# Kernel tuning notes

Hardware: AMD Instinct MI355X
Metric: run time of the kernel (lower is better)

Reference implementation:

```python
import jax, jax.numpy as jnp
import numpy as np

B, S, D, H, DK = 2, 2048, 2048, 16, 128
ALIBI_SLOPE = 8.0
NEG = -1e9  # finite stand-in for -inf so gradients stay finite


def setup_inputs() -> dict:
    key = jax.random.key(0)
    ks = jax.random.split(key, 8)
    states = jax.random.normal(ks[0], (B, S, D), jnp.float32)
    # causal ALiBi-style additive bias: -(i-j) for j<=i else very negative
    pos = jnp.arange(S)
    dist = pos[None, :] - pos[:, None]  # j - i
    bias = jnp.where(dist <= 0, dist.astype(jnp.float32), NEG)
    bias_mask = jnp.broadcast_to(bias[None], (B, S, S))
    # per-head scale: exp2(-((h+1)*slope/H))
    head_scale = jnp.exp2(-((jnp.arange(H) + 1.0) * ALIBI_SLOPE / H)).astype(jnp.float32)
    init = lambda k, shp: jax.random.normal(k, shp, jnp.float32) * (shp[-1] ** -0.5)
    return {
        'states': states,
        'bias_mask': bias_mask,
        'head_scale': head_scale,
        'Wq': init(ks[1], (D, D)), 'bq': jnp.zeros((D,), jnp.float32),
        'Wk': init(ks[2], (D, D)), 'bk': jnp.zeros((D,), jnp.float32),
        'Wv': init(ks[3], (D, D)), 'bv': jnp.zeros((D,), jnp.float32),
        'Wg': init(ks[4], (H, D)), 'bg': jnp.zeros((H,), jnp.float32),
        'Wo': init(ks[5], (D, D)), 'bo': jnp.zeros((D,), jnp.float32),
    }


def reference(states, bias_mask, head_scale, Wq, bq, Wk, bk, Wv, bv, Wg, bg, Wo, bo):
    b, s, d = states.shape
    key_scale = DK ** -0.5
    proj = lambda x, W, bias: x @ W.T + bias
    # [b,s,d] -> [b,h,s,dk]
    q = proj(states, Wq, bq).reshape(b, s, H, DK).transpose(0, 2, 1, 3)
    k = proj(states, Wk, bk).reshape(b, s, H, DK).transpose(0, 2, 1, 3)
    v = proj(states, Wv, bv).reshape(b, s, H, DK).transpose(0, 2, 1, 3)
    # additive per-head ALiBi bias: [b,1,s,s] * [1,h,1,1]
    bias = bias_mask[:, None, :, :] * head_scale[None, :, None, None]
    scores = jnp.einsum('bhqd,bhkd->bhqk', q, k) * key_scale + bias
    attn = jax.nn.softmax(scores, axis=-1)
    o = jnp.einsum('bhqk,bhkd->bhqd', attn, v).transpose(0, 2, 1, 3)  # [b,s,h,dk]
    g = jax.nn.sigmoid(proj(states, Wg, bg))  # [b,s,h]
    o = o * g[..., None]
    return proj(o.reshape(b, s, d), Wo, bo)
```

## Files before the change

kernel.cpp:

```cpp
#include <hip/hip_runtime.h>

#define SEQ  2048
#define NROW 4096
#define KDIM 2048
#define NH   16
#define DKH  128
#define CSUB 20.0f
#define LOG2E 1.44269504088896f

typedef unsigned int u32;
typedef unsigned short u16;
typedef __attribute__((ext_vector_type(8))) __bf16 bf16x8;
typedef __attribute__((ext_vector_type(4))) float f32x4;
typedef __attribute__((ext_vector_type(4))) u16 u16x4;

struct alignas(16) U4 { u32 x, y, z, w; };

__device__ __forceinline__ u16 f2bf(float f) {
  u32 u = __builtin_bit_cast(u32, f);
  u32 r = (u + 0x7fffu + ((u >> 16) & 1u)) >> 16;
  return (u16)r;
}
__device__ __forceinline__ u16 f2bf_n(float f) {
  __bf16 h = (__bf16)f;
  return __builtin_bit_cast(u16, h);
}
__device__ __forceinline__ bf16x8 asb(U4 v) { return __builtin_bit_cast(bf16x8, v); }
__device__ __forceinline__ float exp2a(float x) {
  float r;
  asm("v_exp_f32 %0, %1" : "=v"(r) : "v"(x));
  return r;
}

__device__ __forceinline__ void gl2lds16(const u16* g, u16* l) {
  __builtin_amdgcn_global_load_lds(
      (const __attribute__((address_space(1))) void*)g,
      (__attribute__((address_space(3))) void*)l, 16, 0, 0);
}

__global__ __launch_bounds__(256)
void cvtk(const float* __restrict__ src, u16* __restrict__ dst, int n)
{
  const int i = (blockIdx.x * 256 + threadIdx.x) * 4;
  if (i < n) {
    f32x4 v = *(const f32x4*)(src + i);
    u16x4 o;
#pragma unroll
    for (int j = 0; j < 4; ++j) o[j] = f2bf_n(v[j]);
    *(u16x4*)(dst + i) = o;
  }
}

__global__ __launch_bounds__(256)
void cvt3k(const float* __restrict__ s0, const float* __restrict__ s1,
           const float* __restrict__ s2, u16* __restrict__ dst, int n)
{
  const float* s = blockIdx.y == 0 ? s0 : (blockIdx.y == 1 ? s1 : s2);
  u16* d = dst + (size_t)blockIdx.y * n;
  const int i = (blockIdx.x * 256 + threadIdx.x) * 4;
  if (i < n) {
    f32x4 v = *(const f32x4*)(s + i);
    u16x4 o;
#pragma unroll
    for (int j = 0; j < 4; ++j) o[j] = f2bf_n(v[j]);
    *(u16x4*)(d + i) = o;
  }
}

__device__ __forceinline__ void stage_ab(const u16* __restrict__ A,
                                         const u16* __restrict__ B,
                                         int m0, int n0, int kk,
                                         u16* Asb, u16* Bsb,
                                         int wave, int gr, int gc)
{
#pragma unroll
  for (int it = 0; it < 2; ++it) {
    const int r0 = wave * 32 + it * 16;
    gl2lds16(A + (size_t)(m0 + r0 + gr) * KDIM + kk + gc, Asb + r0 * 32);
    gl2lds16(B + (size_t)(n0 + r0 + gr) * KDIM + kk + gc, Bsb + r0 * 32);
  }
}

__global__ __launch_bounds__(256, 2)
void qkvg(const u16* __restrict__ A, const u16* __restrict__ B,
          const float* __restrict__ bq, const float* __restrict__ bk,
          const float* __restrict__ bv, u16* __restrict__ Qw,
          u16* __restrict__ Kw, u16* __restrict__ Vw)
{
  __shared__ alignas(16) u16 As[2][128 * 32];
  __shared__ alignas(16) u16 Bs[2][128 * 32];
  const int tid = threadIdx.x;
  const int lane = tid & 63, wave = tid >> 6;
  const int wm = wave >> 1, wn = wave & 1;
  const int l15 = lane & 15, quad = lane >> 4;
  const int m0 = blockIdx.y * 128, n0 = blockIdx.x * 128;

  f32x4 acc[4][4];
#pragma unroll
  for (int i = 0; i < 4; ++i)
#pragma unroll
    for (int j = 0; j < 4; ++j) acc[i][j] = {0.f, 0.f, 0.f, 0.f};

  const int gr = lane >> 2;
  const int gc = (lane & 3) * 8;

  stage_ab(A, B, m0, n0, 0, As[0], Bs[0], wave, gr, gc);

  const int NKI = KDIM / 32;
  for (int ki = 0; ki < NKI; ++ki) {
    const int cb = ki & 1;
    __syncthreads();
    if (ki + 1 < NKI)
      stage_ab(A, B, m0, n0, (ki + 1) * 32, As[cb ^ 1], Bs[cb ^ 1], wave, gr, gc);
    U4 af[4], bg[4];
#pragma unroll
    for (int t = 0; t < 4; ++t) {
      af[t] = *(const U4*)(As[cb] + (wm * 64 + t * 16 + l15) * 32 + quad * 8);
      bg[t] = *(const U4*)(Bs[cb] + (wn * 64 + t * 16 + l15) * 32 + quad * 8);
    }
#pragma unroll
    for (int mt = 0; mt < 4; ++mt)
#pragma unroll
      for (int nt = 0; nt < 4; ++nt)
        acc[mt][nt] = __builtin_amdgcn_mfma_f32_16x16x32_bf16(
            asb(af[mt]), asb(bg[nt]), acc[mt][nt], 0, 0, 0);
  }

  const int seg = n0 >> 11;
  const float* bp = seg == 0 ? bq : (seg == 1 ? bk : bv);
  u16* Cq = seg == 0 ? Qw : Kw;

#pragma unroll
  for (int mt = 0; mt < 4; ++mt) {
    const int rowb = m0 + wm * 64 + mt * 16 + quad * 4;
    const int b = rowb >> 11, srow = rowb & (SEQ - 1);
#pragma unroll
    for (int nt = 0; nt < 4; ++nt) {
      const int col6 = n0 + wn * 64 + nt * 16 + l15;
      const int col = col6 & 2047;
      const int h = col >> 7, dk = col & 127;
      const float bvl = bp[col];
      if (seg == 2) {
        u16x4 pk;
#pragma unroll
        for (int r = 0; r < 4; ++r) pk[r] = f2bf_n(acc[mt][nt][r] + bvl);
        const size_t idx = ((size_t)(b * NH + h) * DKH + dk) * SEQ + srow;
        *(u16x4*)(Vw + idx) = pk;
      } else {
#pragma unroll
        for (int r = 0; r < 4; ++r) {
          const size_t idx = ((size_t)(b * NH + h) * SEQ + (srow + r)) * DKH + dk;
          Cq[idx] = f2bf_n(acc[mt][nt][r] + bvl);
        }
      }
    }
  }
}

__global__ __launch_bounds__(256, 2)
void gemm_bt(const u16* __restrict__ A, const u16* __restrict__ B,
             const float* __restrict__ bias, float* __restrict__ Cf)
{
  __shared__ alignas(16) u16 As[2][128 * 32];
  __shared__ alignas(16) u16 Bs[2][128 * 32];
  const int tid = threadIdx.x;
  const int lane = tid & 63, wave = tid >> 6;
  const int wm = wave >> 1, wn = wave & 1;
  const int l15 = lane & 15, quad = lane >> 4;
  const int m0 = blockIdx.y * 128, n0 = blockIdx.x * 128;

  f32x4 acc[4][4];
#pragma unroll
  for (int i = 0; i < 4; ++i)
#pragma unroll
    for (int j = 0; j < 4; ++j) acc[i][j] = {0.f, 0.f, 0.f, 0.f};

  const int gr = lane >> 2;
  const int gc = (lane & 3) * 8;

  stage_ab(A, B, m0, n0, 0, As[0], Bs[0], wave, gr, gc);

  const int NKI = KDIM / 32;
  for (int ki = 0; ki < NKI; ++ki) {
    const int cb = ki & 1;
    __syncthreads();
    if (ki + 1 < NKI)
      stage_ab(A, B, m0, n0, (ki + 1) * 32, As[cb ^ 1], Bs[cb ^ 1], wave, gr, gc);
    U4 af[4], bg[4];
#pragma unroll
    for (int t = 0; t < 4; ++t) {
      af[t] = *(const U4*)(As[cb] + (wm * 64 + t * 16 + l15) * 32 + quad * 8);
      bg[t] = *(const U4*)(Bs[cb] + (wn * 64 + t * 16 + l15) * 32 + quad * 8);
    }
#pragma unroll
    for (int mt = 0; mt < 4; ++mt)
#pragma unroll
      for (int nt = 0; nt < 4; ++nt)
        acc[mt][nt] = __builtin_amdgcn_mfma_f32_16x16x32_bf16(
            asb(af[mt]), asb(bg[nt]), acc[mt][nt], 0, 0, 0);
  }

#pragma unroll
  for (int mt = 0; mt < 4; ++mt) {
    const int rowb = m0 + wm * 64 + mt * 16 + quad * 4;
#pragma unroll
    for (int nt = 0; nt < 4; ++nt) {
      const int col = n0 + wn * 64 + nt * 16 + l15;
      const float bv = bias[col];
#pragma unroll
      for (int r = 0; r < 4; ++r)
        Cf[(size_t)(rowb + r) * KDIM + col] = acc[mt][nt][r] + bv;
    }
  }
}

__global__ __launch_bounds__(256)
void gateg(const u16* __restrict__ X, const float* __restrict__ Wg,
           const float* __restrict__ bg, float* __restrict__ G)
{
  __shared__ float red[4][16][16];
  const int tid = threadIdx.x;
  const int lane = tid & 63, wave = tid >> 6;
  const int l15 = lane & 15, quad = lane >> 4;
  const int m0 = blockIdx.x * 16;

  const u16*  Xp = X + (size_t)(m0 + l15) * KDIM + wave * 512 + quad * 8;
  const float* Wp = Wg + (size_t)l15 * KDIM + wave * 512 + quad * 8;

  f32x4 acc = {0.f, 0.f, 0.f, 0.f};
#pragma unroll
  for (int kk = 0; kk < 512; kk += 32) {
    U4 a = *(const U4*)(Xp + kk);
    f32x4 w0 = *(const f32x4*)(Wp + kk);
    f32x4 w1 = *(const f32x4*)(Wp + kk + 4);
    U4 bw;
    bw.x = (u32)f2bf_n(w0[0]) | ((u32)f2bf_n(w0[1]) << 16);
    bw.y = (u32)f2bf_n(w0[2]) | ((u32)f2bf_n(w0[3]) << 16);
    bw.z = (u32)f2bf_n(w1[0]) | ((u32)f2bf_n(w1[1]) << 16);
    bw.w = (u32)f2bf_n(w1[2]) | ((u32)f2bf_n(w1[3]) << 16);
    acc = __builtin_amdgcn_mfma_f32_16x16x32_bf16(asb(a), asb(bw), acc, 0, 0, 0);
  }
#pragma unroll
  for (int r = 0; r < 4; ++r) red[wave][quad * 4 + r][l15] = acc[r];
  __syncthreads();
  const int row = tid >> 4, head = tid & 15;
  float s = bg[head];
#pragma unroll
  for (int w = 0; w < 4; ++w) s += red[w][row][head];
  G[(size_t)(m0 + row) * NH + head] = 1.f / (1.f + __expf(-s));
}

__device__ __forceinline__ void stage_kv(const u16* __restrict__ Kh,
                                         const u16* __restrict__ Vh,
                                         int kk, u16* Ksb, u16* Vsb,
                                         int wave, int lane)
{
  const int rK = lane >> 4, cK = lane & 15;
  const int rV = lane >> 3, cV = lane & 7;
#pragma unroll
  for (int j = 0; j < 4; ++j) {
    const int r0k = wave * 16 + j * 4;
    const int xk = ((j & 1) << 2) | rK;
    gl2lds16(Kh + (size_t)(kk + r0k + rK) * DKH + ((cK ^ xk) * 8),
             Ksb + r0k * 128);
    const int r0v = wave * 32 + j * 8;
    gl2lds16(Vh + (size_t)(r0v + rV) * SEQ + kk + ((cV ^ rV) * 8),
             Vsb + r0v * 64);
  }
}

__global__ __launch_bounds__(256, 2)
void attnk(const u16* __restrict__ Q, const u16* __restrict__ Km,
           const u16* __restrict__ Vt, const float* __restrict__ hsc,
           const float* __restrict__ G, u16* __restrict__ O)
{
  __shared__ alignas(16) u16 Ks[2][64 * 128];
  __shared__ alignas(16) u16 Vs[2][128 * 64];
  __shared__ alignas(16) u16 Ps[4][16 * 72];
  const int tid = threadIdx.x;
  const int lane = tid & 63, wave = tid >> 6;
  const int l15 = lane & 15, quad = lane >> 4;
  const int l7x = l15 & 7;
  const int qt = 31 - blockIdx.y, bh = blockIdx.x;
  const int b = bh >> 4, h = bh & 15;
  const size_t hoff = (size_t)bh * SEQ * DKH;
  const u16* Qh = Q + hoff;
  const u16* Kh = Km + hoff;
  const u16* Vh = Vt + hoff;
  const float hs2 = hsc[h] * LOG2E;
  const float ks2 = 0.08838834764831845f * LOG2E;
  const float csub2 = CSUB * LOG2E;
  const float dstep = 64.0f * hs2;

  const int q0 = qt * 64 + wave * 16;
  const int ntile = qt + 1;

  U4 aq[4];
#pragma unroll
  for (int c = 0; c < 4; ++c)
    aq[c] = *(const U4*)(Qh + (size_t)(q0 + l15) * DKH + c * 32 + quad * 8);

  float base[4][4];
#pragma unroll
  for (int r = 0; r < 4; ++r) {
    const int i = q0 + quad * 4 + r;
#pragma unroll
    for (int nt = 0; nt < 4; ++nt)
      base[r][nt] = (float)(nt * 16 + l15 - i) * hs2 - csub2;
  }

  f32x4 oacc[8];
#pragma unroll
  for (int c = 0; c < 8; ++c) oacc[c] = {0.f, 0.f, 0.f, 0.f};
  float l_lane[4] = {0.f, 0.f, 0.f, 0.f};

  stage_kv(Kh, Vh, 0, Ks[0], Vs[0], wave, lane);

  for (int t = 0; t < ntile; ++t) {
    const int kk = t * 64;
    const int cb = t & 1;
    __syncthreads();
    if (t + 1 < ntile)
      stage_kv(Kh, Vh, kk + 64, Ks[cb ^ 1], Vs[cb ^ 1], wave, lane);

    f32x4 sf[4];
#pragma unroll
    for (int nt = 0; nt < 4; ++nt) {
      f32x4 s = {0.f, 0.f, 0.f, 0.f};
#pragma unroll
      for (int c = 0; c < 4; ++c) {
        U4 bk = *(const U4*)(Ks[cb] + (nt * 16 + l15) * 128 +
                             (((c * 4 + quad) ^ l7x) * 8));
        s = __builtin_amdgcn_mfma_f32_16x16x32_bf16(asb(aq[c]), asb(bk), s, 0, 0, 0);
      }
      sf[nt] = s;
    }

    u16* Pw = &Ps[wave][0];
    const float tf = (float)t;
    if (t + 1 < ntile) {
#pragma unroll
      for (int r = 0; r < 4; ++r) {
#pragma unroll
        for (int nt = 0; nt < 4; ++nt) {
          const float p = exp2a(fmaf(sf[nt][r], ks2, fmaf(tf, dstep, base[r][nt])));
          l_lane[r] += p;
          Pw[(quad * 4 + r) * 72 + nt * 16 + l15] = f2bf_n(p);
        }
      }
    } else {
#pragma unroll
      for (int r = 0; r < 4; ++r) {
        const int i = q0 + quad * 4 + r;
#pragma unroll
        for (int nt = 0; nt < 4; ++nt) {
          const int j = kk + nt * 16 + l15;
          float p = 0.f;
          if (j <= i)
            p = exp2a(fmaf(sf[nt][r], ks2, fmaf(tf, dstep, base[r][nt])));
          l_lane[r] += p;
          Pw[(quad * 4 + r) * 72 + nt * 16 + l15] = f2bf_n(p);
        }
      }
    }
    asm volatile("s_waitcnt lgkmcnt(0)" ::: "memory");
    __builtin_amdgcn_sched_barrier(0);
    U4 pf0 = *(const U4*)(Pw + l15 * 72 + quad * 8);
    U4 pf1 = *(const U4*)(Pw + l15 * 72 + 32 + quad * 8);
#pragma unroll
    for (int c = 0; c < 8; ++c) {
      U4 bv0 = *(const U4*)(Vs[cb] + (c * 16 + l15) * 64 + ((quad ^ l7x) * 8));
      U4 bv1 = *(const U4*)(Vs[cb] + (c * 16 + l15) * 64 + (((quad + 4) ^ l7x) * 8));
      oacc[c] = __builtin_amdgcn_mfma_f32_16x16x32_bf16(asb(pf0), asb(bv0), oacc[c], 0, 0, 0);
      oacc[c] = __builtin_amdgcn_mfma_f32_16x16x32_bf16(asb(pf1), asb(bv1), oacc[c], 0, 0, 0);
    }
  }

  float sc[4];
#pragma unroll
  for (int r = 0; r < 4; ++r) {
#pragma unroll
    for (int d = 1; d < 16; d <<= 1)
      l_lane[r] += __shfl_xor(l_lane[r], d, 64);
    const int i = q0 + quad * 4 + r;
    sc[r] = G[(size_t)(b * SEQ + i) * NH + h] / l_lane[r];
  }

  __syncthreads();
  u16* OL = &Ks[0][0] + wave * 2112;
#pragma unroll
  for (int c = 0; c < 8; ++c)
#pragma unroll
    for (int r = 0; r < 4; ++r)
      OL[(quad * 4 + r) * 132 + c * 16 + l15] = f2bf_n(oacc[c][r] * sc[r]);
  __syncthreads();
#pragma unroll
  for (int o = 0; o < 4; ++o) {
    const int row = o * 4 + quad;
    U4 val = *(const U4*)(OL + row * 132 + l15 * 8);
    *(U4*)(O + ((size_t)(b * SEQ + q0 + row) * NH + h) * DKH + l15 * 8) = val;
  }
}

extern "C" void kernel_launch(void* const* d_in, const int* in_sizes, int n_in,
                              void* d_out, int out_size, void* d_ws, size_t ws_size,
                              hipStream_t stream)
{
  const float* states = (const float*)d_in[0];
  const float* hscale = (const float*)d_in[2];
  const float* Wq = (const float*)d_in[3];
  const float* bq = (const float*)d_in[4];
  const float* Wk = (const float*)d_in[5];
  const float* bk = (const float*)d_in[6];
  const float* Wv = (const float*)d_in[7];
  const float* bv = (const float*)d_in[8];
  const float* Wg = (const float*)d_in[9];
  const float* bg = (const float*)d_in[10];
  const float* Wo = (const float*)d_in[11];
  const float* bo = (const float*)d_in[12];
  float* out = (float*)d_out;

  char* ws = (char*)d_ws;
  const size_t MB = 1024 * 1024;
  u16* S16  = (u16*)(ws);
  u16* Qw   = (u16*)(ws + 16 * MB);
  u16* Kw   = (u16*)(ws + 32 * MB);
  u16* Vw   = (u16*)(ws + 48 * MB);
  u16* W16  = (u16*)(ws + 64 * MB);
  u16* Ow   = (u16*)(ws + 64 * MB);
  u16* Wo16 = (u16*)(ws + 80 * MB);
  float* Gw = out;

  const int NW = KDIM * KDIM;
  const int NS = NROW * KDIM;
  dim3 blk(256);

  cvtk<<<dim3(NS / 1024), blk, 0, stream>>>(states, S16, NS);
  gateg<<<dim3(NROW / 16), blk, 0, stream>>>(S16, Wg, bg, Gw);
  cvt3k<<<dim3(NW / 1024, 3), blk, 0, stream>>>(Wq, Wk, Wv, W16, NW);
  qkvg<<<dim3(48, 32), blk, 0, stream>>>(S16, W16, bq, bk, bv, Qw, Kw, Vw);
  attnk<<<dim3(32, 32), blk, 0, stream>>>(Qw, Kw, Vw, hscale, Gw, Ow);
  cvtk<<<dim3(NW / 1024), blk, 0, stream>>>(Wo, Wo16, NW);
  gemm_bt<<<dim3(16, 32), blk, 0, stream>>>(Ow, Wo16, bo, out);
}
```

Measured before the change: 427.6 us.

## Enlarge QKV GEMM tiles to 256x256x64 with swizzled LDS and deeper prefetch

Rewrites the fused QKV projection GEMM to use 512-thread blocks with 256x256 output tiles and a K-step of 64. Global-to-LDS loads go into XOR-swizzled layouts to avoid bank conflicts, with two stages in flight tracked by explicit vmcnt waits and raw barriers. MFMA sections run under raised wave priority. Separately, the output-projection gemm_bt is reverted to a single-buffered loop with sync before and after each stage, which may slow that kernel. The larger tile uses much more LDS (128KB) and more registers, which limits occupancy.

```diff
diff --git a/kernel.cpp b/kernel.cpp
--- a/kernel.cpp
+++ b/kernel.cpp
@@ -67,6 +67,113 @@
   }
 }
 
+__global__ __launch_bounds__(512, 2)
+void qkvg(const u16* __restrict__ A, const u16* __restrict__ B,
+          const float* __restrict__ bq, const float* __restrict__ bk,
+          const float* __restrict__ bv, u16* __restrict__ Qw,
+          u16* __restrict__ Kw, u16* __restrict__ Vw)
+{
+  __shared__ alignas(16) u16 As[2][256 * 64];
+  __shared__ alignas(16) u16 Bs[2][256 * 64];
+  const int tid = threadIdx.x;
+  const int lane = tid & 63, wave = tid >> 6;
+  const int wm = wave >> 2, wn = wave & 3;
+  const int l15 = lane & 15, quad = lane >> 4;
+  const int l7 = l15 & 7;
+  const int m0 = blockIdx.y * 256, n0 = blockIdx.x * 256;
+
+  const int srow = wave * 8 + (lane >> 3);
+  const int scol = ((lane & 7) ^ (lane >> 3)) * 8;
+
+  f32x4 acc[8][4];
+#pragma unroll
+  for (int i = 0; i < 8; ++i)
+#pragma unroll
+    for (int j = 0; j < 4; ++j) acc[i][j] = {0.f, 0.f, 0.f, 0.f};
+
+#define QSTAGE(kt, buf)                                                      \
+  do {                                                                       \
+    const int koff_ = (kt) * 64;                                             \
+    _Pragma("unroll")                                                        \
+    for (int j = 0; j < 4; ++j) {                                            \
+      gl2lds16(A + (size_t)(m0 + j * 64 + srow) * KDIM + koff_ + scol,       \
+               &As[buf][(j * 64 + wave * 8) * 64]);                          \
+      gl2lds16(B + (size_t)(n0 + j * 64 + srow) * KDIM + koff_ + scol,       \
+               &Bs[buf][(j * 64 + wave * 8) * 64]);                          \
+    }                                                                        \
+  } while (0)
+
+  QSTAGE(0, 0);
+  QSTAGE(1, 1);
+
+  const int NT = KDIM / 64;
+  for (int kt = 0; kt < NT; ++kt) {
+    const int cb = kt & 1;
+    if (kt + 1 < NT) asm volatile("s_waitcnt vmcnt(8)" ::: "memory");
+    else             asm volatile("s_waitcnt vmcnt(0)" ::: "memory");
+    asm volatile("s_barrier" ::: "memory");
+
+    U4 bf[4][2];
+#pragma unroll
+    for (int nf = 0; nf < 4; ++nf)
+#pragma unroll
+      for (int kf = 0; kf < 2; ++kf)
+        bf[nf][kf] = *(const U4*)(&Bs[cb][(wn * 64 + nf * 16 + l15) * 64 +
+                                          (((kf * 4 + quad) ^ l7) * 8)]);
+    __builtin_amdgcn_s_setprio(1);
+#pragma unroll
+    for (int p = 0; p < 4; ++p) {
+      U4 af[2][2];
+#pragma unroll
+      for (int mi = 0; mi < 2; ++mi)
+#pragma unroll
+        for (int kf = 0; kf < 2; ++kf)
+          af[mi][kf] = *(const U4*)(&As[cb][(wm * 128 + (p * 2 + mi) * 16 + l15) * 64 +
+                                            (((kf * 4 + quad) ^ l7) * 8)]);
+#pragma unroll
+      for (int mi = 0; mi < 2; ++mi)
+#pragma unroll
+        for (int nf = 0; nf < 4; ++nf)
+#pragma unroll
+          for (int kf = 0; kf < 2; ++kf)
+            acc[p * 2 + mi][nf] = __builtin_amdgcn_mfma_f32_16x16x32_bf16(
+                asb(af[mi][kf]), asb(bf[nf][kf]), acc[p * 2 + mi][nf], 0, 0, 0);
+    }
+    __builtin_amdgcn_s_setprio(0);
+    asm volatile("s_barrier" ::: "memory");
+    if (kt + 2 < NT) QSTAGE(kt + 2, cb);
+  }
+#undef QSTAGE
+
+  const int seg = n0 >> 11;
+  const float* bp = seg == 0 ? bq : (seg == 1 ? bk : bv);
+  u16* Cq = seg == 0 ? Qw : Kw;
+
+#pragma unroll
+  for (int mf = 0; mf < 8; ++mf) {
+    const int rowb = m0 + wm * 128 + mf * 16 + quad * 4;
+    const int b = rowb >> 11, sr = rowb & (SEQ - 1);
+#pragma unroll
+    for (int nf = 0; nf < 4; ++nf) {
+      const int col6 = n0 + wn * 64 + nf * 16 + l15;
+      const int col = col6 & 2047;
+      const int h = col >> 7, dk = col & 127;
+      const float bvl = bp[col];
+      if (seg == 2) {
+        u16x4 pk;
+#pragma unroll
+        for (int r = 0; r < 4; ++r) pk[r] = f2bf_n(acc[mf][nf][r] + bvl);
+        *(u16x4*)(Vw + ((size_t)(b * NH + h) * DKH + dk) * SEQ + sr) = pk;
+      } else {
+#pragma unroll
+        for (int r = 0; r < 4; ++r)
+          Cq[((size_t)(b * NH + h) * SEQ + (sr + r)) * DKH + dk] =
+              f2bf_n(acc[mf][nf][r] + bvl);
+      }
+    }
+  }
+}
+
 __device__ __forceinline__ void stage_ab(const u16* __restrict__ A,
                                          const u16* __restrict__ B,
                                          int m0, int n0, int kk,
@@ -82,13 +189,11 @@
 }
 
 __global__ __launch_bounds__(256, 2)
-void qkvg(const u16* __restrict__ A, const u16* __restrict__ B,
-          const float* __restrict__ bq, const float* __restrict__ bk,
-          const float* __restrict__ bv, u16* __restrict__ Qw,
-          u16* __restrict__ Kw, u16* __restrict__ Vw)
-{
-  __shared__ alignas(16) u16 As[2][128 * 32];
-  __shared__ alignas(16) u16 Bs[2][128 * 32];
+void gemm_bt(const u16* __restrict__ A, const u16* __restrict__ B,
+             const float* __restrict__ bias, float* __restrict__ Cf)
+{
+  __shared__ alignas(16) u16 As[128 * 32];
+  __shared__ alignas(16) u16 Bs[128 * 32];
   const int tid = threadIdx.x;
   const int lane = tid & 63, wave = tid >> 6;
   const int wm = wave >> 1, wn = wave & 1;
@@ -104,19 +209,14 @@
   const int gr = lane >> 2;
   const int gc = (lane & 3) * 8;
 
-  stage_ab(A, B, m0, n0, 0, As[0], Bs[0], wave, gr, gc);
-
-  const int NKI = KDIM / 32;
-  for (int ki = 0; ki < NKI; ++ki) {
-    const int cb = ki & 1;
+  for (int kk = 0; kk < KDIM; kk += 32) {
+    stage_ab(A, B, m0, n0, kk, As, Bs, wave, gr, gc);
     __syncthreads();
-    if (ki + 1 < NKI)
-      stage_ab(A, B, m0, n0, (ki + 1) * 32, As[cb ^ 1], Bs[cb ^ 1], wave, gr, gc);
     U4 af[4], bg[4];
 #pragma unroll
     for (int t = 0; t < 4; ++t) {
-      af[t] = *(const U4*)(As[cb] + (wm * 64 + t * 16 + l15) * 32 + quad * 8);
-      bg[t] = *(const U4*)(Bs[cb] + (wn * 64 + t * 16 + l15) * 32 + quad * 8);
+      af[t] = *(const U4*)(As + (wm * 64 + t * 16 + l15) * 32 + quad * 8);
+      bg[t] = *(const U4*)(Bs + (wn * 64 + t * 16 + l15) * 32 + quad * 8);
     }
 #pragma unroll
     for (int mt = 0; mt < 4; ++mt)
@@ -124,80 +224,7 @@
       for (int nt = 0; nt < 4; ++nt)
         acc[mt][nt] = __builtin_amdgcn_mfma_f32_16x16x32_bf16(
             asb(af[mt]), asb(bg[nt]), acc[mt][nt], 0, 0, 0);
-  }
-
-  const int seg = n0 >> 11;
-  const float* bp = seg == 0 ? bq : (seg == 1 ? bk : bv);
-  u16* Cq = seg == 0 ? Qw : Kw;
-
-#pragma unroll
-  for (int mt = 0; mt < 4; ++mt) {
-    const int rowb = m0 + wm * 64 + mt * 16 + quad * 4;
-    const int b = rowb >> 11, srow = rowb & (SEQ - 1);
-#pragma unroll
-    for (int nt = 0; nt < 4; ++nt) {
-      const int col6 = n0 + wn * 64 + nt * 16 + l15;
-      const int col = col6 & 2047;
-      const int h = col >> 7, dk = col & 127;
-      const float bvl = bp[col];
-      if (seg == 2) {
-        u16x4 pk;
-#pragma unroll
-        for (int r = 0; r < 4; ++r) pk[r] = f2bf_n(acc[mt][nt][r] + bvl);
-        const size_t idx = ((size_t)(b * NH + h) * DKH + dk) * SEQ + srow;
-        *(u16x4*)(Vw + idx) = pk;
-      } else {
-#pragma unroll
-        for (int r = 0; r < 4; ++r) {
-          const size_t idx = ((size_t)(b * NH + h) * SEQ + (srow + r)) * DKH + dk;
-          Cq[idx] = f2bf_n(acc[mt][nt][r] + bvl);
-        }
-      }
-    }
-  }
-}
-
-__global__ __launch_bounds__(256, 2)
-void gemm_bt(const u16* __restrict__ A, const u16* __restrict__ B,
-             const float* __restrict__ bias, float* __restrict__ Cf)
-{
-  __shared__ alignas(16) u16 As[2][128 * 32];
-  __shared__ alignas(16) u16 Bs[2][128 * 32];
-  const int tid = threadIdx.x;
-  const int lane = tid & 63, wave = tid >> 6;
-  const int wm = wave >> 1, wn = wave & 1;
-  const int l15 = lane & 15, quad = lane >> 4;
-  const int m0 = blockIdx.y * 128, n0 = blockIdx.x * 128;
-
-  f32x4 acc[4][4];
-#pragma unroll
-  for (int i = 0; i < 4; ++i)
-#pragma unroll
-    for (int j = 0; j < 4; ++j) acc[i][j] = {0.f, 0.f, 0.f, 0.f};
-
-  const int gr = lane >> 2;
-  const int gc = (lane & 3) * 8;
-
-  stage_ab(A, B, m0, n0, 0, As[0], Bs[0], wave, gr, gc);
-
-  const int NKI = KDIM / 32;
-  for (int ki = 0; ki < NKI; ++ki) {
-    const int cb = ki & 1;
     __syncthreads();
-    if (ki + 1 < NKI)
-      stage_ab(A, B, m0, n0, (ki + 1) * 32, As[cb ^ 1], Bs[cb ^ 1], wave, gr, gc);
-    U4 af[4], bg[4];
-#pragma unroll
-    for (int t = 0; t < 4; ++t) {
-      af[t] = *(const U4*)(As[cb] + (wm * 64 + t * 16 + l15) * 32 + quad * 8);
-      bg[t] = *(const U4*)(Bs[cb] + (wn * 64 + t * 16 + l15) * 32 + quad * 8);
-    }
-#pragma unroll
-    for (int mt = 0; mt < 4; ++mt)
-#pragma unroll
-      for (int nt = 0; nt < 4; ++nt)
-        acc[mt][nt] = __builtin_amdgcn_mfma_f32_16x16x32_bf16(
-            asb(af[mt]), asb(bg[nt]), acc[mt][nt], 0, 0, 0);
   }
 
 #pragma unroll
@@ -438,7 +465,7 @@
   cvtk<<<dim3(NS / 1024), blk, 0, stream>>>(states, S16, NS);
   gateg<<<dim3(NROW / 16), blk, 0, stream>>>(S16, Wg, bg, Gw);
   cvt3k<<<dim3(NW / 1024, 3), blk, 0, stream>>>(Wq, Wk, Wv, W16, NW);
-  qkvg<<<dim3(48, 32), blk, 0, stream>>>(S16, W16, bq, bk, bv, Qw, Kw, Vw);
+  qkvg<<<dim3(24, 16), dim3(512), 0, stream>>>(S16, W16, bq, bk, bv, Qw, Kw, Vw);
   attnk<<<dim3(32, 32), blk, 0, stream>>>(Qw, Kw, Vw, hscale, Gw, Ow);
   cvtk<<<dim3(NW / 1024), blk, 0, stream>>>(Wo, Wo16, NW);
   gemm_bt<<<dim3(16, 32), blk, 0, stream>>>(Ow, Wo16, bo, out);
```

Result: no change. 426.2 us (-0.3%).
